# Kernel optimization log

Measured on AMD Instinct MI355X. Metric: run time of the kernel, lower is better.

Reference implementation:

```python
import jax, jax.numpy as jnp
import numpy as np
import functools

N, D, R, E, L, C, MAXDEG = 40000, 128, 3, 640000, 2, 40, 512
BN_EPS = 1e-5


def setup_inputs():
    ks = iter(jax.random.split(jax.random.key(0), 40))
    nrm = lambda s, sc=0.05: jax.random.normal(next(ks), s, dtype=jnp.float32) * sc
    x = jax.random.normal(next(ks), (N, D), dtype=jnp.float32)
    edge_indices = jax.random.randint(next(ks), (R, 2, E), 0, N, dtype=jnp.int32)
    out_emb = nrm((L, MAXDEG, D)).at[:, 0].set(0.0)  # padding_idx=0 -> zero row
    in_emb = nrm((L, MAXDEG, D)).at[:, 0].set(0.0)
    return dict(
        x=x, edge_indices=edge_indices,
        W_src=nrm((L, D, D)), b_src=nrm((L, D)),
        W_dst=nrm((L, D, D)), b_dst=nrm((L, D)),
        W_outf=nrm((L, D)), b_outf=nrm((L,)),
        W_inf=nrm((L, D)), b_inf=nrm((L,)),
        W_fc=nrm((L, D, D)), b_fc=nrm((L, D)),
        bn_gamma=jnp.ones((L, D), jnp.float32), bn_beta=jnp.zeros((L, D), jnp.float32),
        out_deg_emb=out_emb, in_deg_emb=in_emb,
        out_mask=jnp.ones((R, N), jnp.float32), out_mask_bias=jnp.zeros((R, N), jnp.float32),
        in_mask=jnp.ones((R, N), jnp.float32), in_mask_bias=jnp.zeros((R, N), jnp.float32),
        alpha=jnp.float32(0.5), tau=jnp.float32(0.0),
        W_lin=nrm((D, C)), b_lin=nrm((C,)),
    )


def _forward(x, W_src, b_src, W_dst, b_dst, W_outf, b_outf, W_inf, b_inf,
             W_fc, b_fc, bn_gamma, bn_beta, out_deg_emb, in_deg_emb,
             out_mask, out_mask_bias, in_mask, in_mask_bias, alpha, tau,
             W_lin, b_lin, edge_indices):
    seg = lambda d, i: jax.ops.segment_sum(d, i, num_segments=N)
    # source builds I with arange(0, N-1): identity with last diagonal entry missing
    i_mask = (jnp.arange(N) < N - 1).astype(jnp.float32)[:, None]

    rel = []
    for r in range(R):
        row, col = edge_indices[r, 0], edge_indices[r, 1]
        ones = jnp.ones(E, jnp.float32)
        out_deg, in_deg = seg(ones, row), seg(ones, col)
        ods = jnp.where(out_deg > 0, 1.0 / jnp.sqrt(jnp.maximum(out_deg, 1.0)), 0.0)
        ids_ = jnp.where(in_deg > 0, 1.0 / jnp.sqrt(jnp.maximum(in_deg, 1.0)), 0.0)
        # 'dir' norm: D_out^{-1/2} A D_in^{-1/2}; the transposed adj shares the same edge weights
        w = ods[row] * ids_[col]
        rel.append((row, col, w,
                    jnp.clip(out_deg, 0, MAXDEG - 1).astype(jnp.int32),
                    jnp.clip(in_deg, 0, MAXDEG - 1).astype(jnp.int32)))

    def spmm(r_, y):  # adj_norm @ y : gather cols, scatter-add to rows
        row, col, w = rel[r_][0], rel[r_][1], rel[r_][2]
        return seg(w[:, None] * y[col], row)

    def spmm_t(r_, y):  # adj_norm^T @ y
        row, col, w = rel[r_][0], rel[r_][1], rel[r_][2]
        return seg(w[:, None] * y[row], col)

    def dirichlet(mm, y):
        x1 = y / (jnp.sum(jnp.abs(y), axis=1, keepdims=True) + 1e-12)  # row_l1_normalize
        x1sq = x1 * x1
        return (i_mask * x1sq + mm(x1sq)) - 2.0 * ((i_mask * x1 + mm(x1)) * x1 - x1sq)

    eff_tau = jnp.exp(tau) + 0.1

    def conv(l, h):
        out = jnp.zeros((N, D), h.dtype)
        cis, cos_ = [], []
        for r in range(R):
            mm = functools.partial(spmm, r)
            mmt = functools.partial(spmm_t, r)
            out_nei, in_nei = mm(h), mmt(h)
            e_out, e_in = dirichlet(mm, h), dirichlet(mmt, h)
            c_out = (-e_out + out_deg_emb[l][rel[r][3]]) @ W_outf[l] + b_outf[l]  # [N]
            c_in = (-e_in + in_deg_emb[l][rel[r][4]]) @ W_inf[l] + b_inf[l]
            cm = jax.nn.softmax(jnp.stack([c_out, c_in], axis=1) / eff_tau, axis=1)  # tau_softmax
            c_out = cm[:, 0] * out_mask[r] + out_mask_bias[r]
            c_in = cm[:, 1] * in_mask[r] + in_mask_bias[r]
            out = out + c_out[:, None] * (out_nei @ W_src[l] + b_src[l]) \
                      + c_in[:, None] * (in_nei @ W_dst[l] + b_dst[l])
            cis.append(c_in)
            cos_.append(c_out)
        out = out / R
        # F.pad(x,(0,dim-x.shape[1])) is a no-op since input_dim == output_dim
        output = out + alpha * (h @ W_fc[l] + b_fc[l])
        mu, var = jnp.mean(output, axis=0), jnp.var(output, axis=0)  # BatchNorm1d (train mode)
        output = (output - mu) / jnp.sqrt(var + BN_EPS) * bn_gamma[l] + bn_beta[l]
        return output, jnp.mean(jnp.stack(cis), 0)[:, None], jnp.mean(jnp.stack(cos_), 0)[:, None]

    pos_h, neg_h = x, x
    pos_hs, neg_hs, gs, cins, couts = [], [], [], [], []
    for l in range(L):
        ph, ci, co = conv(l, pos_h)
        ph = jax.nn.relu(ph)  # jumping_knowledge truthy -> relu every layer; dropout p=0
        perm = jax.random.permutation(jax.random.key(100 + l), N)  # torch.randperm
        nh, _, _ = conv(l, neg_h[perm])
        nh = jax.nn.relu(nh)
        pos_h, neg_h = ph, nh
        pos_hs.append(ph)
        neg_hs.append(nh)
        gs.append(jnp.mean(ph, axis=0, keepdims=True))
        cins.append(ci)
        couts.append(co)
    c_ins = jnp.mean(jnp.stack(cins), 0)
    c_outs = jnp.mean(jnp.stack(couts), 0)
    jk = functools.reduce(jnp.maximum, pos_hs)  # JumpingKnowledge mode='max'
    logp = jax.nn.log_softmax(jk @ W_lin + b_lin, axis=1)
    return (logp, c_ins, c_outs, *pos_hs, *neg_hs, *gs)


def reference(x, edge_indices, W_src, b_src, W_dst, b_dst, W_outf, b_outf,
              W_inf, b_inf, W_fc, b_fc, bn_gamma, bn_beta, out_deg_emb,
              in_deg_emb, out_mask, out_mask_bias, in_mask, in_mask_bias,
              alpha, tau, W_lin, b_lin):
    return _forward(x, W_src, b_src, W_dst, b_dst, W_outf, b_outf, W_inf, b_inf,
                    W_fc, b_fc, bn_gamma, bn_beta, out_deg_emb, in_deg_emb,
                    out_mask, out_mask_bias, in_mask, in_mask_bias, alpha, tau,
                    W_lin, b_lin, edge_indices)
```

## Files before the change

### kernel.cpp

```cpp
#include <hip/hip_runtime.h>

constexpr int Nn = 40000;
constexpr int Dd = 128;
constexpr int Rr = 3;
constexpr int Ee = 640000;
constexpr int Ll = 2;
constexpr int Cc = 40;
constexpr int MAXD = 512;
constexpr float BN_EPS = 1e-5f;

constexpr int RB_ELEMS = 1024;
constexpr int RB_NB = (Nn + RB_ELEMS - 1) / RB_ELEMS;
constexpr int RB_BINS = 256;

constexpr int HR_BINS = 13334;
constexpr int HR_PAD = 13344;
constexpr int HR_SB = 16;
constexpr int HR_CHUNK = (Ee + HR_SB - 1) / HR_SB;

__device__ __forceinline__ unsigned rotl32(unsigned x, int d) { return (x << d) | (x >> (32 - d)); }

__device__ void threefry2x32(unsigned k0, unsigned k1, unsigned c0, unsigned c1,
                             unsigned& o0, unsigned& o1) {
  unsigned ks2 = k0 ^ k1 ^ 0x1BD11BDAu;
  unsigned x0 = c0 + k0, x1 = c1 + k1;
#define TFR4(a,b,c,d2) \
  x0 += x1; x1 = rotl32(x1,a);  x1 ^= x0; \
  x0 += x1; x1 = rotl32(x1,b);  x1 ^= x0; \
  x0 += x1; x1 = rotl32(x1,c);  x1 ^= x0; \
  x0 += x1; x1 = rotl32(x1,d2); x1 ^= x0;
  TFR4(13,15,26,6);  x0 += k1;  x1 += ks2 + 1u;
  TFR4(17,29,16,24); x0 += ks2; x1 += k0 + 2u;
  TFR4(13,15,26,6);  x0 += k0;  x1 += k1 + 3u;
  TFR4(17,29,16,24); x0 += k1;  x1 += ks2 + 4u;
  TFR4(13,15,26,6);  x0 += ks2; x1 += k0 + 5u;
#undef TFR4
  o0 = x0; o1 = x1;
}

__global__ void k_genkeys(unsigned* __restrict__ keys, unsigned seed, int rounds,
                          int* __restrict__ vout, int doIota) {
  int i = blockIdx.x * blockDim.x + threadIdx.x;
  if (i >= Nn) return;
  unsigned k0 = 0u, k1 = seed, sk0 = 0u, sk1 = 0u;
  for (int rd = 0; rd < rounds; rd++) {
    unsigned a0, a1, b0, b1;
    threefry2x32(k0, k1, 0u, 0u, a0, a1);
    threefry2x32(k0, k1, 0u, 1u, b0, b1);
    sk0 = b0; sk1 = b1;
    k0 = a0; k1 = a1;
  }
  unsigned o0, o1;
  threefry2x32(sk0, sk1, 0u, (unsigned)i, o0, o1);
  keys[i] = o0 ^ o1;
  if (doIota) vout[i] = i;
}

__global__ void k_rhist(const unsigned* __restrict__ keys, int* __restrict__ hist, int shift) {
  __shared__ int lh[RB_BINS];
  int t = threadIdx.x;
  lh[t] = 0;
  __syncthreads();
  int base = blockIdx.x * RB_ELEMS;
  for (int i = t; i < RB_ELEMS; i += 256) {
    int g = base + i;
    if (g < Nn) atomicAdd(&lh[(keys[g] >> shift) & 255], 1);
  }
  __syncthreads();
  hist[t * RB_NB + blockIdx.x] = lh[t];
}

__device__ void scan_body(const int* cnt, int* off, int n, int items) {
  int t = threadIdx.x;
  int lo = t * items, hi = min(lo + items, n);
  int s = 0;
  for (int i = lo; i < hi; i++) s += cnt[i];
  int lane = t & 63, wid = t >> 6;
  int sc = s;
#pragma unroll
  for (int o = 1; o < 64; o <<= 1) {
    int v = __shfl_up(sc, o);
    if (lane >= o) sc += v;
  }
  __shared__ int wsum[16], woff[16];
  if (lane == 63) wsum[wid] = sc;
  __syncthreads();
  if (t == 0) {
    int a = 0;
    for (int w = 0; w < 16; w++) { woff[w] = a; a += wsum[w]; }
    off[n] = a;
  }
  __syncthreads();
  int run = woff[wid] + sc - s;
  for (int i = lo; i < hi; i++) {
    int v = cnt[i];
    off[i] = run;
    run += v;
  }
}

__global__ __launch_bounds__(1024) void k_scanN(const int* __restrict__ cnt, int* __restrict__ off,
                                                int n, int items) {
  scan_body(cnt, off, n, items);
}

__global__ __launch_bounds__(1024) void k_scan6(const int* __restrict__ odeg, const int* __restrict__ ideg,
                                                int* __restrict__ csr_off, int* __restrict__ csc_off) {
  int b = blockIdx.x;
  const int* cnt = (b < 3) ? (odeg + b * Nn) : (ideg + (b - 3) * Nn);
  int* off = (b < 3) ? (csr_off + b * (Nn + 1)) : (csc_off + (b - 3) * (Nn + 1));
  scan_body(cnt, off, Nn, (Nn + 1023) / 1024);
}

__global__ void k_rscatter(const unsigned* __restrict__ keys, const int* __restrict__ vals,
                           const int* __restrict__ scanned, int shift,
                           unsigned* __restrict__ okeys, int* __restrict__ ovals) {
  __shared__ int running[RB_BINS];
  __shared__ int wcount[4][RB_BINS];
  __shared__ int dbase[RB_BINS];
  int t = threadIdx.x;
  int lane = t & 63, w = t >> 6;
  running[t] = 0;
  dbase[t] = scanned[t * RB_NB + blockIdx.x];
  int base = blockIdx.x * RB_ELEMS;
  for (int rnd = 0; rnd < 4; rnd++) {
#pragma unroll
    for (int q = 0; q < 4; q++) wcount[q][t] = 0;
    __syncthreads();
    int g = base + rnd * 256 + t;
    bool valid = g < Nn;
    unsigned key = valid ? keys[g] : 0u;
    int d = (key >> shift) & 255;
    unsigned long long bb = __ballot(valid);
    unsigned long long mask = bb;
#pragma unroll
    for (int k = 0; k < 8; k++) {
      bool b = (d >> k) & 1;
      unsigned long long tt = __ballot(b && valid);
      mask &= b ? tt : ~tt;
    }
    mask &= bb;
    int riw = __popcll(mask & ((1ull << lane) - 1ull));
    int cnt_ = __popcll(mask);
    if (valid && riw == 0) wcount[w][d] = cnt_;
    __syncthreads();
    if (valid) {
      int prior = 0;
#pragma unroll
      for (int ww = 0; ww < 4; ww++) if (ww < w) prior += wcount[ww][d];
      int gp = dbase[d] + running[d] + prior + riw;
      okeys[gp] = key;
      ovals[gp] = vals[g];
    }
    __syncthreads();
    running[t] += wcount[0][t] + wcount[1][t] + wcount[2][t] + wcount[3][t];
    __syncthreads();
  }
}

__global__ void k_permrows(const float* __restrict__ src, const int* __restrict__ perm,
                           float* __restrict__ dst) {
  int row = blockIdx.x * 8 + (threadIdx.x >> 5);
  int lane = threadIdx.x & 31;
  if (row >= Nn) return;
  int p = perm[row];
  ((float4*)(dst + (size_t)row * Dd))[lane] = ((const float4*)(src + (size_t)p * Dd))[lane];
}

__global__ __launch_bounds__(256) void k_hist2(const int* __restrict__ ei, int* __restrict__ partials) {
  __shared__ int lh[HR_BINS];
  int bid = blockIdx.x;
  int sb = bid % HR_SB;
  int range = (bid / HR_SB) % 3;
  int j = bid / (3 * HR_SB);
  int rel = j >> 1, which = j & 1;
  const int* src = ei + (size_t)rel * 2 * Ee + (size_t)which * Ee;
  int lo = range * HR_BINS;
  for (int i = threadIdx.x; i < HR_BINS; i += 256) lh[i] = 0;
  __syncthreads();
  int e0 = sb * HR_CHUNK, e1 = min(e0 + HR_CHUNK, Ee);
  for (int e = e0 + threadIdx.x; e < e1; e += 256) {
    int v = src[e] - lo;
    if (v >= 0 && v < HR_BINS) atomicAdd(&lh[v], 1);
  }
  __syncthreads();
  int* dst = partials + (size_t)bid * HR_PAD;
  for (int i = threadIdx.x; i < HR_BINS; i += 256) dst[i] = lh[i];
}

__global__ void k_hreduce(const int* __restrict__ partials, int* __restrict__ odeg,
                          int* __restrict__ ideg) {
  int idx = blockIdx.x * 256 + threadIdx.x;
  if (idx >= 6 * Nn) return;
  int j = idx / Nn, bin = idx - j * Nn;
  int range = bin / HR_BINS, off = bin - range * HR_BINS;
  const int* p = partials + (size_t)((j * 3 + range) * HR_SB) * HR_PAD + off;
  int sum = 0;
#pragma unroll
  for (int b = 0; b < HR_SB; b++) sum += p[(size_t)b * HR_PAD];
  int rel = j >> 1;
  (j & 1 ? ideg : odeg)[rel * Nn + bin] = sum;
}

__global__ void k_degnorm(const int* __restrict__ odeg, const int* __restrict__ ideg,
                          float* __restrict__ ods, float* __restrict__ ids,
                          int* __restrict__ odix, int* __restrict__ idix) {
  int idx = blockIdx.x * blockDim.x + threadIdx.x;
  if (idx >= Rr * Nn) return;
  int od = odeg[idx], id_ = ideg[idx];
  ods[idx] = od > 0 ? 1.0f / sqrtf((float)od) : 0.0f;
  ids[idx] = id_ > 0 ? 1.0f / sqrtf((float)id_) : 0.0f;
  odix[idx] = od < MAXD - 1 ? od : MAXD - 1;
  idix[idx] = id_ < MAXD - 1 ? id_ : MAXD - 1;
}

__global__ void k_copycur3(const int* __restrict__ csr_off, const int* __restrict__ csc_off,
                           int* __restrict__ cur_out, int* __restrict__ cur_in) {
  int i = blockIdx.x * 256 + threadIdx.x;
  if (i >= 3 * Nn) return;
  int r = i / Nn, n = i - r * Nn;
  cur_out[i] = csr_off[r * (Nn + 1) + n];
  cur_in[i] = csc_off[r * (Nn + 1) + n];
}

__global__ void k_fill3(const int* __restrict__ ei, int* __restrict__ cur_out,
                        int* __restrict__ cur_in,
                        int* __restrict__ csr_col, int* __restrict__ csc_row) {
  int idx = blockIdx.x * 256 + threadIdx.x;
  if (idx >= 3 * Ee) return;
  int r = idx / Ee, e = idx - r * Ee;
  const int* base = ei + (size_t)r * 2 * Ee;
  int rw = base[e], cl = base[Ee + e];
  int po = atomicAdd(&cur_out[r * Nn + rw], 1);
  int pi = atomicAdd(&cur_in[r * Nn + cl], 1);
  csr_col[(size_t)r * Ee + po] = cl;
  csc_row[(size_t)r * Ee + pi] = rw;
}

__global__ void k_rowscalar(const float* __restrict__ h, const float* __restrict__ Wfo,
                            const float* __restrict__ Wfi, float4* __restrict__ aux) {
  int wid = (blockIdx.x * blockDim.x + threadIdx.x) >> 6;
  int lane = threadIdx.x & 63;
  if (wid >= Nn) return;
  float2 a = ((const float2*)(h + (size_t)wid * Dd))[lane];
  float2 wo = ((const float2*)Wfo)[lane];
  float2 wi = ((const float2*)Wfi)[lane];
  float l1 = fabsf(a.x) + fabsf(a.y);
  float so = a.x * a.x * wo.x + a.y * a.y * wo.y;
  float si = a.x * a.x * wi.x + a.y * a.y * wi.y;
#pragma unroll
  for (int o = 32; o; o >>= 1) {
    l1 += __shfl_xor(l1, o);
    so += __shfl_xor(so, o);
    si += __shfl_xor(si, o);
  }
  if (lane == 0) {
    float ri = 1.0f / (l1 + 1e-12f);
    aux[wid] = make_float4(ri, ri * ri * so, ri * ri * si, 0.f);
  }
}

__global__ void k_lut(const float* __restrict__ eo, const float* __restrict__ ei_,
                      const float* __restrict__ Wfo, const float* __restrict__ Wfi,
                      float* __restrict__ luto, float* __restrict__ luti) {
  int wid = (blockIdx.x * blockDim.x + threadIdx.x) >> 6;
  int lane = threadIdx.x & 63;
  if (wid >= MAXD) return;
  float2 a = ((const float2*)(eo + (size_t)wid * Dd))[lane];
  float2 b = ((const float2*)(ei_ + (size_t)wid * Dd))[lane];
  float2 wo = ((const float2*)Wfo)[lane];
  float2 wi = ((const float2*)Wfi)[lane];
  float so = a.x * wo.x + a.y * wo.y;
  float si = b.x * wi.x + b.y * wi.y;
#pragma unroll
  for (int o = 32; o; o >>= 1) { so += __shfl_xor(so, o); si += __shfl_xor(si, o); }
  if (lane == 0) { luto[wid] = so; luti[wid] = si; }
}

__global__ __launch_bounds__(512) void k_csrdir3(
    const int* __restrict__ csr_off, const int* __restrict__ csr_col,
    const int* __restrict__ csc_off, const int* __restrict__ csc_row,
    const float* __restrict__ ods_r, const float* __restrict__ ids_r,
    const float4* __restrict__ aux, const float* __restrict__ h,
    const float* __restrict__ Wfo, const float* __restrict__ Wfi,
    const float* __restrict__ luto, const float* __restrict__ luti,
    const int* __restrict__ odix, const int* __restrict__ idix,
    const float* __restrict__ bo, const float* __restrict__ bi,
    const float* __restrict__ taup,
    const float* __restrict__ omask, const float* __restrict__ omaskb,
    const float* __restrict__ imask, const float* __restrict__ imaskb,
    float* __restrict__ Tout, float* __restrict__ Tin,
    float* __restrict__ sco, float* __restrict__ sci,
    float* __restrict__ co_acc, float* __restrict__ ci_acc,
    int first, int is_pos) {
  __shared__ float lq[8], lp[8], lc[8];
  int t = threadIdx.x;
  int wv = t >> 6, lane = t & 63;
  int dir = wv >> 2;
  int n = blockIdx.x * 4 + (wv & 3);
  const int* off = dir ? csc_off : csr_off;
  const int* nbr = dir ? csc_row : csr_col;
  const float* scn = dir ? ods_r : ids_r;
  float a_self = (dir ? ids_r : ods_r)[n];
  const float* Wf = dir ? Wfi : Wfo;
  int s0 = off[n], s1 = off[n + 1];
  int hl = lane & 31, half = lane >> 5;
  float4 wf4 = ((const float4*)Wf)[hl];
  float4 hn4 = ((const float4*)(h + (size_t)n * Dd))[hl];
  float rn = aux[n].x;
  float4 s = make_float4(0.f, 0.f, 0.f, 0.f);
  float4 pa = make_float4(0.f, 0.f, 0.f, 0.f);
  float qacc = 0.f;
  for (int base = s0; base < s1; base += 64) {
    int eidx = base + lane;
    bool valid = eidx < s1;
    int mi = valid ? nbr[eidx] : 0;
    float4 av = valid ? aux[mi] : make_float4(0.f, 0.f, 0.f, 0.f);
    float scv = valid ? scn[mi] : 0.f;
    float qsel = dir ? av.z : av.y;
    int cnt = min(64, s1 - base);
    for (int j = half; j < cnt; j += 2) {
      int m = __shfl(mi, j);
      float sc = __shfl(scv, j);
      float rm = __shfl(av.x, j);
      float qv = __shfl(qsel, j);
      float w = a_self * sc;
      float wrm = w * rm;
      float4 hv = ((const float4*)(h + (size_t)m * Dd))[hl];
      s.x += w * hv.x; s.y += w * hv.y; s.z += w * hv.z; s.w += w * hv.w;
      pa.x += wrm * hv.x; pa.y += wrm * hv.y; pa.z += wrm * hv.z; pa.w += wrm * hv.w;
      qacc += w * qv;
    }
  }
  s.x += __shfl_xor(s.x, 32); s.y += __shfl_xor(s.y, 32);
  s.z += __shfl_xor(s.z, 32); s.w += __shfl_xor(s.w, 32);
  pa.x += __shfl_xor(pa.x, 32); pa.y += __shfl_xor(pa.y, 32);
  pa.z += __shfl_xor(pa.z, 32); pa.w += __shfl_xor(pa.w, 32);
  qacc += __shfl_xor(qacc, 32);
  float pd = rn * (hn4.x * wf4.x * pa.x + hn4.y * wf4.y * pa.y +
                   hn4.z * wf4.z * pa.z + hn4.w * wf4.w * pa.w);
#pragma unroll
  for (int o = 16; o; o >>= 1) pd += __shfl_xor(pd, o);
  if (lane == 0) { lq[wv] = qacc; lp[wv] = pd; }
  __syncthreads();
  if (t < 4) {
    int nn = blockIdx.x * 4 + t;
    float Qo_ = lq[t], Po_ = lp[t], Qi_ = lq[4 + t], Pi_ = lp[4 + t];
    float4 a2 = aux[nn];
    float im = (nn < Nn - 1) ? 1.0f : 0.0f;
    float so_ = luto[odix[nn]] + bo[0] - (Qo_ - 2.0f * Po_ + (2.0f - im) * a2.y);
    float si_ = luti[idix[nn]] + bi[0] - (Qi_ - 2.0f * Pi_ + (2.0f - im) * a2.z);
    float tt = expf(taup[0]) + 0.1f;
    float aa = so_ / tt, bb = si_ / tt;
    float mm = fmaxf(aa, bb);
    float ea = expf(aa - mm), eb = expf(bb - mm);
    float inv = 1.0f / (ea + eb);
    float co = ea * inv * omask[nn] + omaskb[nn];
    float ci = eb * inv * imask[nn] + imaskb[nn];
    lc[t] = co; lc[4 + t] = ci;
    if (first) { sco[nn] = co; sci[nn] = ci; }
    else       { sco[nn] += co; sci[nn] += ci; }
    if (is_pos) { co_acc[nn] += co; ci_acc[nn] += ci; }
  }
  __syncthreads();
  float c = lc[wv];
  if (lane < 32) {
    float* T = dir ? Tin : Tout;
    size_t o = (size_t)n * Dd;
    float4 v = make_float4(c * s.x, c * s.y, c * s.z, c * s.w);
    if (!first) {
      float4 old = ((const float4*)(T + o))[hl];
      v.x += old.x; v.y += old.y; v.z += old.z; v.w += old.w;
    }
    ((float4*)(T + o))[hl] = v;
  }
}

__global__ __launch_bounds__(256) void k_gemmconv(
    const float* __restrict__ Tout, const float* __restrict__ Tin, const float* __restrict__ h,
    const float* __restrict__ Wsrc, const float* __restrict__ Wdst, const float* __restrict__ Wfc,
    const float* __restrict__ bsrc, const float* __restrict__ bdst, const float* __restrict__ bfc,
    const float* __restrict__ sco, const float* __restrict__ sci,
    const float* __restrict__ alphap, float* __restrict__ pre) {
  __shared__ float Asm[64][36];
  __shared__ float Bsm[32][132];
  int t = threadIdx.x;
  int rg = t >> 5, cg = t & 31;
  int m0 = blockIdx.x * 64;
  int arow = t >> 2, aq = t & 3;
  float alpha = alphap[0];
  float acc[8][4];
#pragma unroll
  for (int r = 0; r < 8; r++)
#pragma unroll
    for (int c = 0; c < 4; c++) acc[r][c] = 0.f;
  for (int kt = 0; kt < 12; kt++) {
    int sec = kt >> 2, kc = (kt & 3) * 32;
    const float* Ap = sec == 0 ? Tout : (sec == 1 ? Tin : h);
    const float* Wp = sec == 0 ? Wsrc : (sec == 1 ? Wdst : Wfc);
    float sA = (sec == 2) ? alpha : (1.0f / (float)Rr);
    __syncthreads();
    {
      const float4* src = (const float4*)(Ap + (size_t)(m0 + arow) * Dd + kc + aq * 8);
      float4 v0 = src[0], v1 = src[1];
      float4* d0 = (float4*)&Asm[arow][aq * 8];
      d0[0] = make_float4(v0.x * sA, v0.y * sA, v0.z * sA, v0.w * sA);
      d0[1] = make_float4(v1.x * sA, v1.y * sA, v1.z * sA, v1.w * sA);
    }
#pragma unroll
    for (int j = 0; j < 4; j++) {
      int idx = t + j * 256;
      int k = idx >> 5, d4 = idx & 31;
      *(float4*)&Bsm[k][d4 * 4] = *(const float4*)(Wp + (size_t)(kc + k) * Dd + d4 * 4);
    }
    __syncthreads();
#pragma unroll
    for (int kk = 0; kk < 32; kk += 4) {
      float4 af[8], bf[4];
#pragma unroll
      for (int r = 0; r < 8; r++) af[r] = *(const float4*)&Asm[rg * 8 + r][kk];
#pragma unroll
      for (int j = 0; j < 4; j++) bf[j] = *(const float4*)&Bsm[kk + j][cg * 4];
#pragma unroll
      for (int r = 0; r < 8; r++) {
        const float* ap = (const float*)&af[r];
#pragma unroll
        for (int j = 0; j < 4; j++) {
          const float* bp = (const float*)&bf[j];
          acc[r][0] += ap[j] * bp[0];
          acc[r][1] += ap[j] * bp[1];
          acc[r][2] += ap[j] * bp[2];
          acc[r][3] += ap[j] * bp[3];
        }
      }
    }
  }
  float4 vb1 = *(const float4*)(bsrc + cg * 4);
  float4 vb2 = *(const float4*)(bdst + cg * 4);
  float4 vbf = *(const float4*)(bfc + cg * 4);
#pragma unroll
  for (int r = 0; r < 8; r++) {
    int row = m0 + rg * 8 + r;
    size_t o = (size_t)row * Dd + cg * 4;
    float s1 = sco[row] * (1.0f / (float)Rr), s2 = sci[row] * (1.0f / (float)Rr);
    float4 v;
    v.x = acc[r][0] + s1 * vb1.x + s2 * vb2.x + alpha * vbf.x;
    v.y = acc[r][1] + s1 * vb1.y + s2 * vb2.y + alpha * vbf.y;
    v.z = acc[r][2] + s1 * vb1.z + s2 * vb2.z + alpha * vbf.z;
    v.w = acc[r][3] + s1 * vb1.w + s2 * vb2.w + alpha * vbf.w;
    *(float4*)(pre + o) = v;
  }
}

__global__ void k_bnstats(const float* __restrict__ pre, float* __restrict__ sums) {
  __shared__ float ls[256], ls2[256];
  int c = threadIdx.x & 127, sub = threadIdx.x >> 7;
  float s = 0.f, s2 = 0.f;
  for (int n = blockIdx.x * 2 + sub; n < Nn; n += gridDim.x * 2) {
    float v = pre[(size_t)n * Dd + c];
    s += v; s2 += v * v;
  }
  ls[threadIdx.x] = s; ls2[threadIdx.x] = s2;
  __syncthreads();
  if (sub == 0) {
    atomicAdd(&sums[c], ls[c] + ls[c + 128]);
    atomicAdd(&sums[c + 128], ls2[c] + ls2[c + 128]);
  }
}

__global__ void k_bnapply(const float* __restrict__ pre, const float* __restrict__ sums,
                          const float* __restrict__ gamma, const float* __restrict__ beta,
                          float* __restrict__ hout, float* __restrict__ gs, int do_gs) {
  __shared__ float ls[256];
  int c = threadIdx.x & 127, sub = threadIdx.x >> 7;
  float mu = sums[c] * (1.0f / (float)Nn);
  float var = sums[c + 128] * (1.0f / (float)Nn) - mu * mu;
  float sc = gamma[c] / sqrtf(var + BN_EPS);
  float bt = beta[c];
  float g = 0.f;
  for (int n = blockIdx.x * 2 + sub; n < Nn; n += gridDim.x * 2) {
    float v = (pre[(size_t)n * Dd + c] - mu) * sc + bt;
    v = fmaxf(v, 0.f);
    hout[(size_t)n * Dd + c] = v;
    g += v;
  }
  if (do_gs) {
    ls[threadIdx.x] = g;
    __syncthreads();
    if (sub == 0) atomicAdd(&gs[c], (ls[c] + ls[c + 128]) * (1.0f / (float)Nn));
  }
}

__global__ void k_cio(const float* __restrict__ ci_acc, const float* __restrict__ co_acc,
                      float* __restrict__ cins, float* __restrict__ couts) {
  int n = blockIdx.x * blockDim.x + threadIdx.x;
  if (n < Nn) {
    cins[n] = ci_acc[n] * (1.0f / (float)(Ll * Rr));
    couts[n] = co_acc[n] * (1.0f / (float)(Ll * Rr));
  }
}

__global__ __launch_bounds__(64) void k_logp(const float* __restrict__ ph0, const float* __restrict__ ph1,
                      const float* __restrict__ Wlin, const float* __restrict__ blin,
                      float* __restrict__ logp) {
  __shared__ float jk[Dd];
  __shared__ float lg[Cc];
  int n = blockIdx.x, t = threadIdx.x;
  for (int d = t; d < Dd; d += 64) jk[d] = fmaxf(ph0[(size_t)n * Dd + d], ph1[(size_t)n * Dd + d]);
  __syncthreads();
  if (t < Cc) {
    float acc = blin[t];
    for (int k = 0; k < Dd; k++) acc += jk[k] * Wlin[k * Cc + t];
    lg[t] = acc;
  }
  __syncthreads();
  float m = -1e30f;
  for (int c = 0; c < Cc; c++) m = fmaxf(m, lg[c]);
  float s = 0.f;
  for (int c = 0; c < Cc; c++) s += expf(lg[c] - m);
  float lse = m + logf(s);
  if (t < Cc) logp[(size_t)n * Cc + t] = lg[t] - lse;
}

extern "C" void kernel_launch(void* const* d_in, const int* in_sizes, int n_in,
                              void* d_out, int out_size, void* d_ws, size_t ws_size,
                              hipStream_t stream) {
  const float* x      = (const float*)d_in[0];
  const int*   ei     = (const int*)d_in[1];
  const float* W_src  = (const float*)d_in[2];
  const float* b_src  = (const float*)d_in[3];
  const float* W_dst  = (const float*)d_in[4];
  const float* b_dst  = (const float*)d_in[5];
  const float* W_outf = (const float*)d_in[6];
  const float* b_outf = (const float*)d_in[7];
  const float* W_inf  = (const float*)d_in[8];
  const float* b_inf  = (const float*)d_in[9];
  const float* W_fc   = (const float*)d_in[10];
  const float* b_fc   = (const float*)d_in[11];
  const float* gamma  = (const float*)d_in[12];
  const float* beta   = (const float*)d_in[13];
  const float* oemb   = (const float*)d_in[14];
  const float* iemb   = (const float*)d_in[15];
  const float* omask  = (const float*)d_in[16];
  const float* omaskb = (const float*)d_in[17];
  const float* imask  = (const float*)d_in[18];
  const float* imaskb = (const float*)d_in[19];
  const float* alphap = (const float*)d_in[20];
  const float* taup   = (const float*)d_in[21];
  const float* Wlin   = (const float*)d_in[22];
  const float* blin   = (const float*)d_in[23];

  float* out   = (float*)d_out;
  float* logp  = out;
  float* cins  = logp + (size_t)Nn * Cc;
  float* couts = cins + Nn;
  float* ph0   = couts + Nn;
  float* ph1   = ph0 + (size_t)Nn * Dd;
  float* nh0   = ph1 + (size_t)Nn * Dd;
  float* nh1   = nh0 + (size_t)Nn * Dd;
  float* gs0   = nh1 + (size_t)Nn * Dd;
  float* gs1   = gs0 + Dd;

  char* p = (char*)d_ws;
  auto alloc = [&](size_t bytes) -> void* {
    void* q = (void*)p;
    p += (bytes + 255) & ~(size_t)255;
    return q;
  };
  float* pre   = (float*)alloc((size_t)Nn * Dd * 4);
  float* Tout  = (float*)alloc((size_t)Nn * Dd * 4);
  float* Tin   = (float*)alloc((size_t)Nn * Dd * 4);
  float* hperm = (float*)alloc((size_t)Nn * Dd * 4);
  int* csr_col = (int*)alloc((size_t)Rr * Ee * 4);
  int* csc_row = (int*)alloc((size_t)Rr * Ee * 4);
  int* csr_off = (int*)alloc((size_t)Rr * (Nn + 1) * 4);
  int* csc_off = (int*)alloc((size_t)Rr * (Nn + 1) * 4);
  int* cur_out = (int*)alloc((size_t)Rr * Nn * 4);
  int* cur_in  = (int*)alloc((size_t)Rr * Nn * 4);
  int* odeg    = (int*)alloc((size_t)Rr * Nn * 4);
  int* ideg    = (int*)alloc((size_t)Rr * Nn * 4);
  float* ods   = (float*)alloc((size_t)Rr * Nn * 4);
  float* ids   = (float*)alloc((size_t)Rr * Nn * 4);
  int* odix    = (int*)alloc((size_t)Rr * Nn * 4);
  int* idix    = (int*)alloc((size_t)Rr * Nn * 4);
  float4* aux  = (float4*)alloc((size_t)Nn * 16);
  float* sco   = (float*)alloc((size_t)Nn * 4 * 2);
  float* sci   = sco + Nn;
  float* coacc = (float*)alloc((size_t)Nn * 4 * 2);
  float* ciacc = coacc + Nn;
  float* luto  = (float*)alloc(MAXD * 4);
  float* luti  = (float*)alloc(MAXD * 4);
  float* bnsum = (float*)alloc(256 * 4);
  unsigned* kbuf0 = (unsigned*)alloc((size_t)Nn * 4);
  unsigned* kbuf1 = (unsigned*)alloc((size_t)Nn * 4);
  int* vbuf0 = (int*)alloc((size_t)Nn * 4);
  int* vbuf1 = (int*)alloc((size_t)Nn * 4);
  int* rhist = (int*)alloc((size_t)(RB_BINS * RB_NB + 1) * 4);
  int* rscan = (int*)alloc((size_t)(RB_BINS * RB_NB + 1) * 4);
  int* partials = (int*)alloc((size_t)(6 * 3 * HR_SB) * HR_PAD * 4);

  k_hist2<<<6 * 3 * HR_SB, 256, 0, stream>>>(ei, partials);
  k_hreduce<<<(6 * Nn + 255) / 256, 256, 0, stream>>>(partials, odeg, ideg);
  k_degnorm<<<(Rr * Nn + 255) / 256, 256, 0, stream>>>(odeg, ideg, ods, ids, odix, idix);
  k_scan6<<<6, 1024, 0, stream>>>(odeg, ideg, csr_off, csc_off);
  k_copycur3<<<(3 * Nn + 255) / 256, 256, 0, stream>>>(csr_off, csc_off, cur_out, cur_in);
  k_fill3<<<(3 * Ee + 255) / 256, 256, 0, stream>>>(ei, cur_out, cur_in, csr_col, csc_row);
  hipMemsetAsync(coacc, 0, (size_t)Nn * 4 * 2, stream);

  auto radix4 = [&]() {
    for (int pass = 0; pass < 4; pass++) {
      const unsigned* ik = (pass & 1) ? kbuf1 : kbuf0;
      const int*      iv = (pass & 1) ? vbuf1 : vbuf0;
      unsigned*       ok = (pass & 1) ? kbuf0 : kbuf1;
      int*            ov = (pass & 1) ? vbuf0 : vbuf1;
      int shift = pass * 8;
      k_rhist<<<RB_NB, 256, 0, stream>>>(ik, rhist, shift);
      k_scanN<<<1, 1024, 0, stream>>>(rhist, rscan, RB_BINS * RB_NB, (RB_BINS * RB_NB + 1023) / 1024);
      k_rscatter<<<RB_NB, 256, 0, stream>>>(ik, iv, rscan, shift, ok, ov);
    }
  };

  auto make_perm = [&](unsigned seed) {
    k_genkeys<<<(Nn + 255) / 256, 256, 0, stream>>>(kbuf0, seed, 1, vbuf0, 1);
    radix4();
    k_genkeys<<<(Nn + 255) / 256, 256, 0, stream>>>(kbuf0, seed, 2, vbuf0, 0);
    radix4();
  };

  auto conv = [&](int l, const float* hin, float* hout, float* gs, int is_pos) {
    const float* Wfo = W_outf + l * Dd;
    const float* Wfi = W_inf + l * Dd;
    k_rowscalar<<<Nn / 4, 256, 0, stream>>>(hin, Wfo, Wfi, aux);
    for (int r = 0; r < Rr; r++) {
      k_csrdir3<<<Nn / 4, 512, 0, stream>>>(csr_off + r * (Nn + 1), csr_col + (size_t)r * Ee,
                                            csc_off + r * (Nn + 1), csc_row + (size_t)r * Ee,
                                            ods + r * Nn, ids + r * Nn, aux, hin, Wfo, Wfi,
                                            luto, luti, odix + r * Nn, idix + r * Nn,
                                            b_outf + l, b_inf + l, taup,
                                            omask + (size_t)r * Nn, omaskb + (size_t)r * Nn,
                                            imask + (size_t)r * Nn, imaskb + (size_t)r * Nn,
                                            Tout, Tin, sco, sci, coacc, ciacc,
                                            r == 0 ? 1 : 0, is_pos);
    }
    k_gemmconv<<<Nn / 64, 256, 0, stream>>>(Tout, Tin, hin,
                                            W_src + (size_t)l * Dd * Dd, W_dst + (size_t)l * Dd * Dd,
                                            W_fc + (size_t)l * Dd * Dd,
                                            b_src + l * Dd, b_dst + l * Dd, b_fc + l * Dd,
                                            sco, sci, alphap, pre);
    hipMemsetAsync(bnsum, 0, 256 * 4, stream);
    k_bnstats<<<256, 256, 0, stream>>>(pre, bnsum);
    if (is_pos) hipMemsetAsync(gs, 0, Dd * 4, stream);
    k_bnapply<<<256, 256, 0, stream>>>(pre, bnsum, gamma + l * Dd, beta + l * Dd, hout, gs, is_pos);
  };

  k_lut<<<MAXD / 4, 256, 0, stream>>>(oemb, iemb, W_outf, W_inf, luto, luti);
  conv(0, x, ph0, gs0, 1);
  make_perm(100u);
  k_permrows<<<Nn / 8, 256, 0, stream>>>(x, vbuf0, hperm);
  conv(0, hperm, nh0, nullptr, 0);

  k_lut<<<MAXD / 4, 256, 0, stream>>>(oemb + (size_t)MAXD * Dd, iemb + (size_t)MAXD * Dd,
                                      W_outf + Dd, W_inf + Dd, luto, luti);
  conv(1, ph0, ph1, gs1, 1);
  make_perm(101u);
  k_permrows<<<Nn / 8, 256, 0, stream>>>(nh0, vbuf0, hperm);
  conv(1, hperm, nh1, nullptr, 0);

  k_cio<<<(Nn + 255) / 256, 256, 0, stream>>>(ciacc, coacc, cins, couts);
  k_logp<<<Nn, 64, 0, stream>>>(ph0, ph1, Wlin, blin, logp);
}
```

Before: 2.606 ms.

## Build CSR/CSC adjacency via packed-key stable radix sort instead of atomic fill

Replaces the atomic-counter fill of CSR/CSC neighbor arrays with packing (src<<16|dst) keys and a two-pass stable 8-bit LSD radix sort on the high 16 bits, per relation and direction. This makes neighbor lists deterministic and sorted by original edge order, removing the heavy random atomics of the fill step. The consumer now extracts the neighbor index from the low 16 bits. This relies on node ids fitting in 16 bits, but N=40000 needs 16 bits only for the neighbor part and the key's high part, so it is fine here. It adds six extra kernel launches and more passes over the edge arrays.

```diff
diff --git a/kernel.cpp b/kernel.cpp
--- a/kernel.cpp
+++ b/kernel.cpp
@@ -12,6 +12,10 @@
 constexpr int RB_ELEMS = 1024;
 constexpr int RB_NB = (Nn + RB_ELEMS - 1) / RB_ELEMS;
 constexpr int RB_BINS = 256;
+
+constexpr int EB_ELEMS = 4096;
+constexpr int EB_NB = (Ee + EB_ELEMS - 1) / EB_ELEMS;
+constexpr int EB_H = 256 * EB_NB;
 
 constexpr int HR_BINS = 13334;
 constexpr int HR_PAD = 13344;
@@ -214,27 +218,84 @@
   idix[idx] = id_ < MAXD - 1 ? id_ : MAXD - 1;
 }
 
-__global__ void k_copycur3(const int* __restrict__ csr_off, const int* __restrict__ csc_off,
-                           int* __restrict__ cur_out, int* __restrict__ cur_in) {
-  int i = blockIdx.x * 256 + threadIdx.x;
-  if (i >= 3 * Nn) return;
-  int r = i / Nn, n = i - r * Nn;
-  cur_out[i] = csr_off[r * (Nn + 1) + n];
-  cur_in[i] = csc_off[r * (Nn + 1) + n];
-}
-
-__global__ void k_fill3(const int* __restrict__ ei, int* __restrict__ cur_out,
-                        int* __restrict__ cur_in,
-                        int* __restrict__ csr_col, int* __restrict__ csc_row) {
+__global__ void k_pack(const int* __restrict__ ei, unsigned* __restrict__ pcsr,
+                       unsigned* __restrict__ pcsc) {
   int idx = blockIdx.x * 256 + threadIdx.x;
   if (idx >= 3 * Ee) return;
   int r = idx / Ee, e = idx - r * Ee;
   const int* base = ei + (size_t)r * 2 * Ee;
-  int rw = base[e], cl = base[Ee + e];
-  int po = atomicAdd(&cur_out[r * Nn + rw], 1);
-  int pi = atomicAdd(&cur_in[r * Nn + cl], 1);
-  csr_col[(size_t)r * Ee + po] = cl;
-  csc_row[(size_t)r * Ee + pi] = rw;
+  unsigned rw = (unsigned)base[e], cl = (unsigned)base[Ee + e];
+  pcsr[idx] = (rw << 16) | cl;
+  pcsc[idx] = (cl << 16) | rw;
+}
+
+__global__ __launch_bounds__(256) void k_ehist(const unsigned* __restrict__ pin,
+                                               int* __restrict__ hist, int shift) {
+  __shared__ int lh[256];
+  int a = blockIdx.x / EB_NB, blk = blockIdx.x % EB_NB;
+  const unsigned* src = pin + (size_t)a * Ee;
+  lh[threadIdx.x] = 0;
+  __syncthreads();
+  int base = blk * EB_ELEMS;
+  for (int i = threadIdx.x; i < EB_ELEMS; i += 256) {
+    int g = base + i;
+    if (g < Ee) atomicAdd(&lh[(src[g] >> shift) & 255], 1);
+  }
+  __syncthreads();
+  hist[(size_t)a * EB_H + threadIdx.x * EB_NB + blk] = lh[threadIdx.x];
+}
+
+__global__ __launch_bounds__(1024) void k_escan6(const int* __restrict__ hist, int* __restrict__ esc) {
+  int a = blockIdx.x;
+  scan_body(hist + (size_t)a * EB_H, esc + (size_t)a * (EB_H + 1), EB_H, (EB_H + 1023) / 1024);
+}
+
+__global__ __launch_bounds__(256) void k_escatter(const unsigned* __restrict__ pin,
+                                                  const int* __restrict__ esc, int shift,
+                                                  unsigned* __restrict__ pout) {
+  __shared__ int running[256];
+  __shared__ int wcount[4][256];
+  __shared__ int dbase[256];
+  int a = blockIdx.x / EB_NB, blk = blockIdx.x % EB_NB;
+  const unsigned* src = pin + (size_t)a * Ee;
+  unsigned* dst = pout + (size_t)a * Ee;
+  int t = threadIdx.x;
+  int lane = t & 63, w = t >> 6;
+  running[t] = 0;
+  dbase[t] = esc[(size_t)a * (EB_H + 1) + t * EB_NB + blk];
+  int base = blk * EB_ELEMS;
+  for (int rnd = 0; rnd < 16; rnd++) {
+#pragma unroll
+    for (int q = 0; q < 4; q++) wcount[q][t] = 0;
+    __syncthreads();
+    int g = base + rnd * 256 + t;
+    bool valid = g < Ee;
+    unsigned key = valid ? src[g] : 0u;
+    int d = (key >> shift) & 255;
+    unsigned long long bb = __ballot(valid);
+    unsigned long long mask = bb;
+#pragma unroll
+    for (int k = 0; k < 8; k++) {
+      bool b = (d >> k) & 1;
+      unsigned long long tt = __ballot(b && valid);
+      mask &= b ? tt : ~tt;
+    }
+    mask &= bb;
+    int riw = __popcll(mask & ((1ull << lane) - 1ull));
+    int cnt_ = __popcll(mask);
+    if (valid && riw == 0) wcount[w][d] = cnt_;
+    __syncthreads();
+    if (valid) {
+      int prior = 0;
+#pragma unroll
+      for (int ww = 0; ww < 4; ww++) if (ww < w) prior += wcount[ww][d];
+      int gp = dbase[d] + running[d] + prior + riw;
+      dst[gp] = key;
+    }
+    __syncthreads();
+    running[t] += wcount[0][t] + wcount[1][t] + wcount[2][t] + wcount[3][t];
+    __syncthreads();
+  }
 }
 
 __global__ void k_rowscalar(const float* __restrict__ h, const float* __restrict__ Wfo,
@@ -278,8 +339,8 @@
 }
 
 __global__ __launch_bounds__(512) void k_csrdir3(
-    const int* __restrict__ csr_off, const int* __restrict__ csr_col,
-    const int* __restrict__ csc_off, const int* __restrict__ csc_row,
+    const int* __restrict__ csr_off, const unsigned* __restrict__ pcsr,
+    const int* __restrict__ csc_off, const unsigned* __restrict__ pcsc,
     const float* __restrict__ ods_r, const float* __restrict__ ids_r,
     const float4* __restrict__ aux, const float* __restrict__ h,
     const float* __restrict__ Wfo, const float* __restrict__ Wfi,
@@ -299,7 +360,7 @@
   int dir = wv >> 2;
   int n = blockIdx.x * 4 + (wv & 3);
   const int* off = dir ? csc_off : csr_off;
-  const int* nbr = dir ? csc_row : csr_col;
+  const unsigned* nbrp = dir ? pcsc : pcsr;
   const float* scn = dir ? ods_r : ids_r;
   float a_self = (dir ? ids_r : ods_r)[n];
   const float* Wf = dir ? Wfi : Wfo;
@@ -314,7 +375,7 @@
   for (int base = s0; base < s1; base += 64) {
     int eidx = base + lane;
     bool valid = eidx < s1;
-    int mi = valid ? nbr[eidx] : 0;
+    int mi = valid ? (int)(pcsr[0], nbrp[eidx] & 0xFFFFu) : 0;
     float4 av = valid ? aux[mi] : make_float4(0.f, 0.f, 0.f, 0.f);
     float scv = valid ? scn[mi] : 0.f;
     float qsel = dir ? av.z : av.y;
@@ -571,12 +632,13 @@
   float* Tout  = (float*)alloc((size_t)Nn * Dd * 4);
   float* Tin   = (float*)alloc((size_t)Nn * Dd * 4);
   float* hperm = (float*)alloc((size_t)Nn * Dd * 4);
-  int* csr_col = (int*)alloc((size_t)Rr * Ee * 4);
-  int* csc_row = (int*)alloc((size_t)Rr * Ee * 4);
+  unsigned* pbuf = (unsigned*)alloc((size_t)6 * Ee * 4);
+  size_t qwords = (size_t)6 * Ee;
+  size_t pwords = (size_t)(6 * 3 * HR_SB) * HR_PAD;
+  unsigned* qbuf = (unsigned*)alloc((qwords > pwords ? qwords : pwords) * 4);
+  int* partials = (int*)qbuf;
   int* csr_off = (int*)alloc((size_t)Rr * (Nn + 1) * 4);
   int* csc_off = (int*)alloc((size_t)Rr * (Nn + 1) * 4);
-  int* cur_out = (int*)alloc((size_t)Rr * Nn * 4);
-  int* cur_in  = (int*)alloc((size_t)Rr * Nn * 4);
   int* odeg    = (int*)alloc((size_t)Rr * Nn * 4);
   int* ideg    = (int*)alloc((size_t)Rr * Nn * 4);
   float* ods   = (float*)alloc((size_t)Rr * Nn * 4);
@@ -597,14 +659,20 @@
   int* vbuf1 = (int*)alloc((size_t)Nn * 4);
   int* rhist = (int*)alloc((size_t)(RB_BINS * RB_NB + 1) * 4);
   int* rscan = (int*)alloc((size_t)(RB_BINS * RB_NB + 1) * 4);
-  int* partials = (int*)alloc((size_t)(6 * 3 * HR_SB) * HR_PAD * 4);
+  int* ehist = (int*)alloc((size_t)6 * EB_H * 4);
+  int* escan = (int*)alloc((size_t)6 * (EB_H + 1) * 4);
 
   k_hist2<<<6 * 3 * HR_SB, 256, 0, stream>>>(ei, partials);
   k_hreduce<<<(6 * Nn + 255) / 256, 256, 0, stream>>>(partials, odeg, ideg);
   k_degnorm<<<(Rr * Nn + 255) / 256, 256, 0, stream>>>(odeg, ideg, ods, ids, odix, idix);
   k_scan6<<<6, 1024, 0, stream>>>(odeg, ideg, csr_off, csc_off);
-  k_copycur3<<<(3 * Nn + 255) / 256, 256, 0, stream>>>(csr_off, csc_off, cur_out, cur_in);
-  k_fill3<<<(3 * Ee + 255) / 256, 256, 0, stream>>>(ei, cur_out, cur_in, csr_col, csc_row);
+  k_pack<<<(3 * Ee + 255) / 256, 256, 0, stream>>>(ei, pbuf, pbuf + (size_t)3 * Ee);
+  k_ehist<<<6 * EB_NB, 256, 0, stream>>>(pbuf, ehist, 16);
+  k_escan6<<<6, 1024, 0, stream>>>(ehist, escan);
+  k_escatter<<<6 * EB_NB, 256, 0, stream>>>(pbuf, escan, 16, qbuf);
+  k_ehist<<<6 * EB_NB, 256, 0, stream>>>(qbuf, ehist, 24);
+  k_escan6<<<6, 1024, 0, stream>>>(ehist, escan);
+  k_escatter<<<6 * EB_NB, 256, 0, stream>>>(qbuf, escan, 24, pbuf);
   hipMemsetAsync(coacc, 0, (size_t)Nn * 4 * 2, stream);
 
   auto radix4 = [&]() {
@@ -632,8 +700,8 @@
     const float* Wfi = W_inf + l * Dd;
     k_rowscalar<<<Nn / 4, 256, 0, stream>>>(hin, Wfo, Wfi, aux);
     for (int r = 0; r < Rr; r++) {
-      k_csrdir3<<<Nn / 4, 512, 0, stream>>>(csr_off + r * (Nn + 1), csr_col + (size_t)r * Ee,
-                                            csc_off + r * (Nn + 1), csc_row + (size_t)r * Ee,
+      k_csrdir3<<<Nn / 4, 512, 0, stream>>>(csr_off + r * (Nn + 1), pbuf + (size_t)r * Ee,
+                                            csc_off + r * (Nn + 1), pbuf + (size_t)(3 + r) * Ee,
                                             ods + r * Nn, ids + r * Nn, aux, hin, Wfo, Wfi,
                                             luto, luti, odix + r * Nn, idix + r * Nn,
                                             b_outf + l, b_inf + l, taup,
```

New measurement: 2.473 ms. 1.05x faster.
